# Performance work log

Measured on AMD Instinct MI355X. Metric: run time of the kernel, lower is better.

The kernel has to match this reference:

```python
import jax, jax.numpy as jnp
import numpy as np

N_NODES = 50000
N_EDGES = 1600000
N_GRAPHS = 2048
DIM = 133
EPS = 1e-5


def gcn_conv(x, W, b, row, col, n_nodes):
    # PyG GCNConv: h = x @ W; add self-loops; sym-normalized scatter-add; + b
    h = x @ W  # [N, D]
    loops = jnp.arange(n_nodes, dtype=row.dtype)
    r = jnp.concatenate([row, loops])
    c = jnp.concatenate([col, loops])
    deg = jax.ops.segment_sum(jnp.ones_like(c, dtype=h.dtype), c, num_segments=n_nodes)
    dinv = jnp.where(deg > 0, jax.lax.rsqrt(deg), 0.0)
    norm = dinv[r] * dinv[c]  # [E+N]
    msg = h[r] * norm[:, None]  # gather + scale
    out = jax.ops.segment_sum(msg, c, num_segments=n_nodes)
    return out + b


def batchnorm_eval(x, gamma, beta, rm, rv):
    return (x - rm) * jax.lax.rsqrt(rv + EPS) * gamma + beta


def setup_inputs() -> dict:
    key = jax.random.key(0)
    ks = jax.random.split(key, 8)
    x = jax.random.normal(ks[0], (N_NODES, DIM), dtype=jnp.float32)
    edge_index = jax.random.randint(ks[1], (2, N_EDGES), 0, N_NODES, dtype=jnp.int64)
    batch = jnp.sort(jax.random.randint(ks[2], (N_NODES,), 0, N_GRAPHS, dtype=jnp.int64))
    s = 1.0 / np.sqrt(DIM)
    W1 = jax.random.uniform(ks[3], (DIM, DIM), jnp.float32, -s, s)
    W2 = jax.random.uniform(ks[4], (DIM, DIM), jnp.float32, -s, s)
    b1 = jnp.zeros((DIM,), jnp.float32)
    b2 = jnp.zeros((DIM,), jnp.float32)
    g1 = jnp.ones((DIM,), jnp.float32); beta1 = jnp.zeros((DIM,), jnp.float32)
    rm1 = jax.random.normal(ks[5], (DIM,), jnp.float32) * 0.1
    rv1 = jnp.ones((DIM,), jnp.float32)
    g2 = jnp.ones((DIM,), jnp.float32); beta2 = jnp.zeros((DIM,), jnp.float32)
    rm2 = jax.random.normal(ks[6], (DIM,), jnp.float32) * 0.1
    rv2 = jnp.ones((DIM,), jnp.float32)
    return {"x": x, "edge_index": edge_index, "batch": batch,
            "W1": W1, "b1": b1, "W2": W2, "b2": b2,
            "g1": g1, "beta1": beta1, "rm1": rm1, "rv1": rv1,
            "g2": g2, "beta2": beta2, "rm2": rm2, "rv2": rv2}


def reference(x, edge_index, batch, W1, b1, W2, b2,
              g1, beta1, rm1, rv1, g2, beta2, rm2, rv2):
    row, col = edge_index[0], edge_index[1]
    h = gcn_conv(x, W1, b1, row, col, N_NODES)
    h = jax.nn.relu(h)
    h = batchnorm_eval(h, g1, beta1, rm1, rv1)  # eval-mode BN; dropout is identity in eval
    h = gcn_conv(h, W2, b2, row, col, N_NODES)
    h = jax.nn.relu(h)
    h = batchnorm_eval(h, g2, beta2, rm2, rv2)
    # global mean pool per graph
    sums = jax.ops.segment_sum(h, batch, num_segments=N_GRAPHS)
    cnts = jax.ops.segment_sum(jnp.ones((N_NODES,), h.dtype), batch, num_segments=N_GRAPHS)
    return sums / jnp.maximum(cnts, 1.0)[:, None]
```

## Files before the change

kernel.cpp:

```cpp
#include <hip/hip_runtime.h>

#define N_NODES  50000
#define N_ROWS   50048
#define N_EDGES  1600000
#define N_GRAPHS 2048
#define DIM      133
#define HMSTR    128
#define HTSTR    8
#define YSTR     160
#define EPSV     1e-5f
#define NRANGE   16
#define RSPAN    3125
#define NSLICE   64
#define BUCKCAP  110000
#define EPB      1563
#define NPN      4

typedef __attribute__((ext_vector_type(8))) short bf16x8;
typedef __attribute__((ext_vector_type(4))) float f32x4;

__device__ __forceinline__ float blo(unsigned u) { return __uint_as_float(u << 16); }
__device__ __forceinline__ float bhi(unsigned u) { return __uint_as_float(u & 0xFFFF0000u); }
__device__ __forceinline__ unsigned short f2bf(float x) {
    unsigned v = __float_as_uint(x);
    return (unsigned short)((v + 0x7FFFu + ((v >> 16) & 1u)) >> 16);
}
__device__ __forceinline__ unsigned packbf(float a, float b) {
    return (unsigned)f2bf(a) | ((unsigned)f2bf(b) << 16);
}


__global__ __launch_bounds__(256) void k_part(const int* __restrict__ row,
                                              const int* __restrict__ col,
                                              int* __restrict__ bcnt,
                                              unsigned* __restrict__ buckets)
{
    __shared__ int cnt[NRANGE];
    __shared__ int cur[NRANGE];
    int e0 = blockIdx.x * EPB;
    if (threadIdx.x < NRANGE) cnt[threadIdx.x] = 0;
    __syncthreads();
    int e1 = min(e0 + EPB, N_EDGES);
    for (int e = e0 + threadIdx.x; e < e1; e += 256)
        atomicAdd(&cnt[col[e] / RSPAN], 1);
    __syncthreads();
    if (threadIdx.x < NRANGE)
        cur[threadIdx.x] = atomicAdd(&bcnt[threadIdx.x], cnt[threadIdx.x]);
    __syncthreads();
    for (int e = e0 + threadIdx.x; e < e1; e += 256) {
        int c = col[e];
        int r = c / RSPAN;
        int p = atomicAdd(&cur[r], 1);
        buckets[(size_t)r * BUCKCAP + p] =
            ((unsigned)row[e] << 12) | (unsigned)(c - r * RSPAN);
    }
}

__global__ __launch_bounds__(256) void k_count2(const unsigned* __restrict__ buckets,
                                                const int* __restrict__ bcnt,
                                                int* __restrict__ deg2)
{
    __shared__ int hist[RSPAN];
    int r = blockIdx.x & (NRANGE - 1);
    int s = blockIdx.x >> 4;
    int lo = r * RSPAN;
    for (int i = threadIdx.x; i < RSPAN; i += 256) hist[i] = 0;
    __syncthreads();
    int n = bcnt[r];
    int chunk = (n + NSLICE - 1) / NSLICE;
    int e0 = s * chunk, e1 = min(e0 + chunk, n);
    const unsigned* b = buckets + (size_t)r * BUCKCAP;
    for (int e = e0 + threadIdx.x; e < e1; e += 256)
        atomicAdd(&hist[b[e] & 0xFFFu], 1);
    __syncthreads();
    for (int i = threadIdx.x; i < RSPAN; i += 256)
        deg2[(size_t)s * N_NODES + lo + i] = hist[i];
}

__device__ __forceinline__ void w2bf_one(const float* __restrict__ W,
                                         unsigned short* __restrict__ Wbf, int idx)
{
    int j    = idx & 7;
    int lane = (idx >> 3) & 63;
    int kc   = (idx >> 9) % 5;
    int t    = idx / (8 * 64 * 5);
    int k = kc * 32 + (lane >> 4) * 8 + j;
    int n = t * 16 + (lane & 15);
    float v = (k < DIM && n < DIM) ? W[k * DIM + n] : 0.f;
    Wbf[idx] = f2bf(v);
}

#define X2BF_BLOCKS 15625

__global__ __launch_bounds__(256) void k_prep(const float* __restrict__ x,
                                              unsigned* __restrict__ Abf,
                                              const float* __restrict__ W1,
                                              const float* __restrict__ W2,
                                              unsigned short* __restrict__ Wbf1,
                                              unsigned short* __restrict__ Wbf2,
                                              const int* __restrict__ batch,
                                              float* __restrict__ inv_cnt)
{
    if (blockIdx.x < X2BF_BLOCKS) {
        int idx = blockIdx.x * 256 + threadIdx.x;
        if (idx >= N_NODES * 80) return;
        int r  = idx / 80;
        int c2 = (idx - r * 80) * 2;
        float a = (c2     < DIM) ? x[(size_t)r * DIM + c2]     : 0.f;
        float b = (c2 + 1 < DIM) ? x[(size_t)r * DIM + c2 + 1] : 0.f;
        Abf[idx] = packbf(a, b);
        return;
    }
    int tid = (blockIdx.x - X2BF_BLOCKS) * 256 + threadIdx.x;
    if (tid < 23040) {
        w2bf_one(W1, Wbf1, tid);
    } else if (tid < 46080) {
        w2bf_one(W2, Wbf2, tid - 23040);
    } else if (tid < 46080 + N_GRAPHS) {
        int g = tid - 46080;
        int a0 = 0, b0 = N_NODES;
        while (a0 < b0) { int m = (a0 + b0) >> 1; if (batch[m] < g) a0 = m + 1; else b0 = m; }
        int a1 = a0, b1 = N_NODES;
        while (a1 < b1) { int m = (a1 + b1) >> 1; if (batch[m] < g + 1) a1 = m + 1; else b1 = m; }
        inv_cnt[g] = 1.0f / (float)max(a1 - a0, 1);
    }
}

__global__ __launch_bounds__(256) void k_scan1(const int* __restrict__ deg2,
                                               float* __restrict__ dinv,
                                               int* __restrict__ offs,
                                               int* __restrict__ bsum)
{
    __shared__ int sd[256];
    int t = threadIdx.x;
    int idx = blockIdx.x * 256 + t;
    int v = 0;
    if (idx < N_NODES) {
        for (int s = 0; s < NSLICE; s++) v += deg2[(size_t)s * N_NODES + idx];
        dinv[idx] = rsqrtf((float)v + 1.0f);
    }
    sd[t] = v; __syncthreads();
    for (int o = 1; o < 256; o <<= 1) {
        int add = (t >= o) ? sd[t - o] : 0;
        __syncthreads();
        sd[t] += add;
        __syncthreads();
    }
    if (idx < N_NODES) offs[idx] = sd[t] - v;
    if (t == 255) bsum[blockIdx.x] = sd[255];
}

__global__ __launch_bounds__(256) void k_scan2(const int* __restrict__ bsum,
                                               int* __restrict__ boff, int nb)
{
    __shared__ int sd[256];
    int t = threadIdx.x;
    int v = (t < nb) ? bsum[t] : 0;
    sd[t] = v; __syncthreads();
    for (int o = 1; o < 256; o <<= 1) {
        int add = (t >= o) ? sd[t - o] : 0;
        __syncthreads();
        sd[t] += add;
        __syncthreads();
    }
    boff[t] = sd[t] - v;
}

__global__ __launch_bounds__(256) void k_scan3C(int* __restrict__ offs,
                                                const int* __restrict__ boff,
                                                int* __restrict__ deg2)
{
    int idx = blockIdx.x * 256 + threadIdx.x;
    if (idx < N_NODES) {
        int off = offs[idx] + boff[blockIdx.x];
        offs[idx] = off;
        int run = off;
        for (int s = 0; s < NSLICE; s++) {
            int d = deg2[(size_t)s * N_NODES + idx];
            deg2[(size_t)s * N_NODES + idx] = run;
            run += d;
        }
    } else if (idx == N_NODES) {
        offs[N_NODES] = N_EDGES;
    }
}

__global__ __launch_bounds__(256) void k_fill2(const unsigned* __restrict__ buckets,
                                               const int* __restrict__ bcnt,
                                               const int* __restrict__ offs2,
                                               const float* __restrict__ dinv,
                                               unsigned* __restrict__ csr)
{
    __shared__ int cur[RSPAN];
    int r = blockIdx.x & (NRANGE - 1);
    int s = blockIdx.x >> 4;
    int lo = r * RSPAN;
    for (int i = threadIdx.x; i < RSPAN; i += 256)
        cur[i] = offs2[(size_t)s * N_NODES + lo + i];
    __syncthreads();
    int n = bcnt[r];
    int chunk = (n + NSLICE - 1) / NSLICE;
    int e0 = s * chunk, e1 = min(e0 + chunk, n);
    const unsigned* b = buckets + (size_t)r * BUCKCAP;
    for (int e = e0 + threadIdx.x; e < e1; e += 256) {
        unsigned v = b[e];
        int src = (int)(v >> 12);
        int p = atomicAdd(&cur[v & 0xFFFu], 1);
        csr[p] = ((unsigned)src << 16) | (unsigned)f2bf(dinv[src]);
    }
}

__global__ __launch_bounds__(256) void k_gemm_mfma(const unsigned short* __restrict__ A,
                                                   const unsigned short* __restrict__ Wbf,
                                                   unsigned short* __restrict__ Hmain,
                                                   unsigned short* __restrict__ Htail, int M)
{
    int wave = threadIdx.x >> 6, lane = threadIdx.x & 63;
    int quad = lane >> 4, l16 = lane & 15;
    int m = blockIdx.x * 64 + wave * 16 + l16;

    const bf16x8* Arow = (const bf16x8*)(A + (size_t)m * YSTR);
    const bf16x8* Bq   = (const bf16x8*)Wbf;

    f32x4 acc[9] = {};
#pragma unroll
    for (int kc = 0; kc < 5; kc++) {
        bf16x8 af = Arow[kc * 4 + quad];
#pragma unroll
        for (int t = 0; t < 9; t++) {
            bf16x8 bfr = Bq[(t * 5 + kc) * 64 + lane];
            acc[t] = __builtin_amdgcn_mfma_f32_16x16x32_bf16(af, bfr, acc[t], 0, 0, 0);
        }
    }

    int gr0 = blockIdx.x * 64 + wave * 16 + quad * 4;
#pragma unroll
    for (int t = 0; t < 9; t++) {
        int c = t * 16 + l16;
#pragma unroll
        for (int reg = 0; reg < 4; reg++) {
            int gr = gr0 + reg;
            if (gr < M) {
                if (c < HMSTR) {
                    Hmain[(size_t)gr * HMSTR + c] = f2bf(acc[t][reg]);
                } else if (c < HMSTR + HTSTR) {
                    float v = (c < DIM) ? acc[t][reg] : 0.f;
                    Htail[(size_t)gr * HTSTR + (c - HMSTR)] = f2bf(v);
                }
            }
        }
    }
}


__device__ __forceinline__ void agg_row(const unsigned short* __restrict__ hmain,
                                        const unsigned short* __restrict__ htail,
                                        const int* __restrict__ offs,
                                        const unsigned* __restrict__ csr,
                                        const float* __restrict__ dinv,
                                        const float* __restrict__ bias,
                                        const float* __restrict__ gam,
                                        const float* __restrict__ bet,
                                        const float* __restrict__ rmean,
                                        const float* __restrict__ rvar,
                                        int node, int lane, int l2,
                                        float& va, float& vb, float& ta, float& tb)
{
    const unsigned* hm = (const unsigned*)hmain;
    const unsigned* ht = (const unsigned*)htail;

    float di = dinv[node];
    unsigned pw0 = hm[((size_t)node << 6) + lane];
    unsigned pw1 = ht[((unsigned)node << 2) + l2];
    float2 a0; a0.x = di * blo(pw0); a0.y = di * bhi(pw0);
    float2 a1; a1.x = di * blo(pw1); a1.y = di * bhi(pw1);

    int s0 = offs[node], s1 = offs[node + 1];
    int e = s0;
    for (; e + 8 <= s1; e += 8) {
        unsigned rec[8];
#pragma unroll
        for (int u = 0; u < 8; u++)
            rec[u] = __builtin_amdgcn_readfirstlane(csr[e + u]);
        unsigned q0[8], q1[8];
#pragma unroll
        for (int u = 0; u < 8; u++) {
            const unsigned* hr = hm + ((size_t)(rec[u] >> 16) << 6);
            const unsigned* tr = ht + ((rec[u] >> 16) << 2);
            q0[u] = hr[lane];
            q1[u] = tr[l2];
        }
#pragma unroll
        for (int u = 0; u < 8; u++) {
            float w = __uint_as_float(rec[u] << 16);
            a0.x += w * blo(q0[u]); a0.y += w * bhi(q0[u]);
            a1.x += w * blo(q1[u]); a1.y += w * bhi(q1[u]);
        }
    }
    for (; e < s1; e++) {
        unsigned rec = __builtin_amdgcn_readfirstlane(csr[e]);
        const unsigned* hr = hm + ((size_t)(rec >> 16) << 6);
        const unsigned* tr = ht + ((rec >> 16) << 2);
        float w = __uint_as_float(rec << 16);
        unsigned q0 = hr[lane];
        unsigned q1 = tr[l2];
        a0.x += w * blo(q0); a0.y += w * bhi(q0);
        a1.x += w * blo(q1); a1.y += w * bhi(q1);
    }

    {
        int c = 2 * lane;
        float v = di * a0.x + bias[c];
        v = fmaxf(v, 0.f);
        va = (v - rmean[c]) * (gam[c] * rsqrtf(rvar[c] + EPSV)) + bet[c];
        int c1 = c + 1;
        v = di * a0.y + bias[c1];
        v = fmaxf(v, 0.f);
        vb = (v - rmean[c1]) * (gam[c1] * rsqrtf(rvar[c1] + EPSV)) + bet[c1];
    }
    ta = 0.f; tb = 0.f;
    if (lane < 4) {
        int c = 128 + 2 * l2;
        if (c < DIM) {
            float v = di * a1.x + bias[c];
            v = fmaxf(v, 0.f);
            ta = (v - rmean[c]) * (gam[c] * rsqrtf(rvar[c] + EPSV)) + bet[c];
        }
        int c1 = c + 1;
        if (c1 < DIM) {
            float v = di * a1.y + bias[c1];
            v = fmaxf(v, 0.f);
            tb = (v - rmean[c1]) * (gam[c1] * rsqrtf(rvar[c1] + EPSV)) + bet[c1];
        }
    }
}

template <bool FINAL>
__global__ __launch_bounds__(256) void k_agg(const unsigned short* __restrict__ hmain,
                                             const unsigned short* __restrict__ htail,
                                             const int* __restrict__ offs,
                                             const unsigned* __restrict__ csr,
                                             const float* __restrict__ dinv,
                                             const float* __restrict__ bias,
                                             const float* __restrict__ gam,
                                             const float* __restrict__ bet,
                                             const float* __restrict__ rmean,
                                             const float* __restrict__ rvar,
                                             unsigned short* __restrict__ y,
                                             const int* __restrict__ batch,
                                             const float* __restrict__ inv_cnt,
                                             float* __restrict__ outp)
{
    int lane = threadIdx.x & 63;
    int l2 = lane & 3;

    if (!FINAL) {
        int node = __builtin_amdgcn_readfirstlane(blockIdx.x * 4 + (threadIdx.x >> 6));
        if (node >= N_NODES) return;
        float va, vb, ta, tb;
        agg_row(hmain, htail, offs, csr, dinv, bias, gam, bet, rmean, rvar,
                node, lane, l2, va, vb, ta, tb);
        ((unsigned*)(y + (size_t)node * YSTR))[lane] = packbf(va, vb);
        if (lane < 16)
            ((unsigned*)(y + (size_t)node * YSTR))[64 + lane] =
                (lane < 4) ? packbf(ta, tb) : 0u;
        return;
    }

    int node0 = __builtin_amdgcn_readfirstlane((blockIdx.x * 4 + (threadIdx.x >> 6)) * NPN);
    if (node0 >= N_NODES) return;
    int nend = min(node0 + NPN, N_NODES);

    float p0x = 0.f, p0y = 0.f, p1x = 0.f, p1y = 0.f;
    int curg = batch[node0];

    for (int node = node0; node < nend; node++) {
        int bg = batch[node];
        if (bg != curg) {
            float ic = inv_cnt[curg];
            int c = 2 * lane;
            atomicAdd(&outp[(size_t)curg * DIM + c],     p0x * ic);
            atomicAdd(&outp[(size_t)curg * DIM + c + 1], p0y * ic);
            if (lane < 4) {
                int ct = 128 + 2 * l2;
                if (ct     < DIM) atomicAdd(&outp[(size_t)curg * DIM + ct],     p1x * ic);
                if (ct + 1 < DIM) atomicAdd(&outp[(size_t)curg * DIM + ct + 1], p1y * ic);
            }
            p0x = p0y = p1x = p1y = 0.f;
            curg = bg;
        }
        float va, vb, ta, tb;
        agg_row(hmain, htail, offs, csr, dinv, bias, gam, bet, rmean, rvar,
                node, lane, l2, va, vb, ta, tb);
        p0x += va; p0y += vb; p1x += ta; p1y += tb;
    }
    {
        float ic = inv_cnt[curg];
        int c = 2 * lane;
        atomicAdd(&outp[(size_t)curg * DIM + c],     p0x * ic);
        atomicAdd(&outp[(size_t)curg * DIM + c + 1], p0y * ic);
        if (lane < 4) {
            int ct = 128 + 2 * l2;
            if (ct     < DIM) atomicAdd(&outp[(size_t)curg * DIM + ct],     p1x * ic);
            if (ct + 1 < DIM) atomicAdd(&outp[(size_t)curg * DIM + ct + 1], p1y * ic);
        }
    }
}


extern "C" void kernel_launch(void* const* d_in, const int* in_sizes, int n_in,
                              void* d_out, int out_size, void* d_ws, size_t ws_size,
                              hipStream_t stream)
{
    const float* x   = (const float*)d_in[0];
    const int*   ei  = (const int*)d_in[1];
    const int*   bat = (const int*)d_in[2];
    const float* W1  = (const float*)d_in[3];
    const float* b1  = (const float*)d_in[4];
    const float* W2  = (const float*)d_in[5];
    const float* b2  = (const float*)d_in[6];
    const float* g1  = (const float*)d_in[7];
    const float* be1 = (const float*)d_in[8];
    const float* rm1 = (const float*)d_in[9];
    const float* rv1 = (const float*)d_in[10];
    const float* g2  = (const float*)d_in[11];
    const float* be2 = (const float*)d_in[12];
    const float* rm2 = (const float*)d_in[13];
    const float* rv2 = (const float*)d_in[14];
    float* outp = (float*)d_out;
    char* ws = (char*)d_ws;

    int*   bcnt    = (int*)  (ws + 0);
    int*   offs    = (int*)  (ws + 200000);
    float* dinv    = (float*)(ws + 400016);
    float* inv_cnt = (float*)(ws + 600016);
    int*   bsum    = (int*)  (ws + 608208);
    int*   boff    = (int*)  (ws + 609232);
    unsigned* csr  = (unsigned*)(ws + 610256);
    unsigned short* Wbf1 = (unsigned short*)(ws + 7010256);
    unsigned short* Wbf2 = (unsigned short*)(ws + 7056336);
    unsigned short* Abf  = (unsigned short*)(ws + 7102416);
    unsigned short* Y1   = Abf;
    unsigned short* Hm   = (unsigned short*)(ws + 23118080);
    unsigned short* Ht   = (unsigned short*)(ws + 35930368);
    unsigned* buckets = (unsigned*)(ws + 23118080);
    int*      deg2    = (int*)    (ws + 30158080);

    hipMemsetAsync(bcnt, 0, 64, stream);
    hipMemsetAsync(d_out, 0, (size_t)out_size * 4, stream);

    const int* row = ei;
    const int* col = ei + N_EDGES;

    int nbl = (N_NODES + 255) / 256;

    k_part  <<<dim3(1024), dim3(256), 0, stream>>>(row, col, bcnt, buckets);
    k_prep  <<<dim3(X2BF_BLOCKS + 189), dim3(256), 0, stream>>>(x, (unsigned*)Abf,
                                                                W1, W2, Wbf1, Wbf2,
                                                                bat, inv_cnt);
    k_count2<<<dim3(NSLICE * NRANGE), dim3(256), 0, stream>>>(buckets, bcnt, deg2);
    k_scan1 <<<dim3(nbl), dim3(256), 0, stream>>>(deg2, dinv, offs, bsum);
    k_scan2 <<<dim3(1),   dim3(256), 0, stream>>>(bsum, boff, nbl);
    k_scan3C<<<dim3(nbl), dim3(256), 0, stream>>>(offs, boff, deg2);
    k_fill2 <<<dim3(NSLICE * NRANGE), dim3(256), 0, stream>>>(buckets, bcnt, deg2, dinv, csr);

    int gbl = N_ROWS / 64;
    k_gemm_mfma<<<dim3(gbl), dim3(256), 0, stream>>>(Abf, Wbf1, Hm, Ht, N_NODES);
    k_agg<false><<<dim3(N_NODES / 4), dim3(256), 0, stream>>>(Hm, Ht, offs, csr, dinv,
                                                              b1, g1, be1, rm1, rv1,
                                                              Y1, nullptr, nullptr, nullptr);
    k_gemm_mfma<<<dim3(gbl), dim3(256), 0, stream>>>(Y1, Wbf2, Hm, Ht, N_NODES);
    int fbl = (N_NODES + 4 * NPN - 1) / (4 * NPN);
    k_agg<true><<<dim3(fbl), dim3(256), 0, stream>>>(Hm, Ht, offs, csr, dinv,
                                                     b2, g2, be2, rm2, rv2,
                                                     nullptr, bat, inv_cnt, outp);
}
```

Before: 322.6 us.

## Replace bucketed two-pass CSR build with direct global-atomic degree count and fill

```diff
diff --git a/kernel.cpp b/kernel.cpp
--- a/kernel.cpp
+++ b/kernel.cpp
@@ -9,12 +9,8 @@
 #define HTSTR    8
 #define YSTR     160
 #define EPSV     1e-5f
-#define NRANGE   16
-#define RSPAN    3125
-#define NSLICE   64
-#define BUCKCAP  110000
-#define EPB      1563
 #define NPN      4
+#define EPB2     782
 
 typedef __attribute__((ext_vector_type(8))) short bf16x8;
 typedef __attribute__((ext_vector_type(4))) float f32x4;
@@ -29,53 +25,6 @@
     return (unsigned)f2bf(a) | ((unsigned)f2bf(b) << 16);
 }
 
-
-__global__ __launch_bounds__(256) void k_part(const int* __restrict__ row,
-                                              const int* __restrict__ col,
-                                              int* __restrict__ bcnt,
-                                              unsigned* __restrict__ buckets)
-{
-    __shared__ int cnt[NRANGE];
-    __shared__ int cur[NRANGE];
-    int e0 = blockIdx.x * EPB;
-    if (threadIdx.x < NRANGE) cnt[threadIdx.x] = 0;
-    __syncthreads();
-    int e1 = min(e0 + EPB, N_EDGES);
-    for (int e = e0 + threadIdx.x; e < e1; e += 256)
-        atomicAdd(&cnt[col[e] / RSPAN], 1);
-    __syncthreads();
-    if (threadIdx.x < NRANGE)
-        cur[threadIdx.x] = atomicAdd(&bcnt[threadIdx.x], cnt[threadIdx.x]);
-    __syncthreads();
-    for (int e = e0 + threadIdx.x; e < e1; e += 256) {
-        int c = col[e];
-        int r = c / RSPAN;
-        int p = atomicAdd(&cur[r], 1);
-        buckets[(size_t)r * BUCKCAP + p] =
-            ((unsigned)row[e] << 12) | (unsigned)(c - r * RSPAN);
-    }
-}
-
-__global__ __launch_bounds__(256) void k_count2(const unsigned* __restrict__ buckets,
-                                                const int* __restrict__ bcnt,
-                                                int* __restrict__ deg2)
-{
-    __shared__ int hist[RSPAN];
-    int r = blockIdx.x & (NRANGE - 1);
-    int s = blockIdx.x >> 4;
-    int lo = r * RSPAN;
-    for (int i = threadIdx.x; i < RSPAN; i += 256) hist[i] = 0;
-    __syncthreads();
-    int n = bcnt[r];
-    int chunk = (n + NSLICE - 1) / NSLICE;
-    int e0 = s * chunk, e1 = min(e0 + chunk, n);
-    const unsigned* b = buckets + (size_t)r * BUCKCAP;
-    for (int e = e0 + threadIdx.x; e < e1; e += 256)
-        atomicAdd(&hist[b[e] & 0xFFFu], 1);
-    __syncthreads();
-    for (int i = threadIdx.x; i < RSPAN; i += 256)
-        deg2[(size_t)s * N_NODES + lo + i] = hist[i];
-}
 
 __device__ __forceinline__ void w2bf_one(const float* __restrict__ W,
                                          unsigned short* __restrict__ Wbf, int idx)
@@ -90,7 +39,10 @@
     Wbf[idx] = f2bf(v);
 }
 
-#define X2BF_BLOCKS 15625
+#define PRB_X 15625
+#define PRB_W 189
+#define PRB_Z 1064
+#define PRB_H 2048
 
 __global__ __launch_bounds__(256) void k_prep(const float* __restrict__ x,
                                               unsigned* __restrict__ Abf,
@@ -99,34 +51,50 @@
                                               unsigned short* __restrict__ Wbf1,
                                               unsigned short* __restrict__ Wbf2,
                                               const int* __restrict__ batch,
-                                              float* __restrict__ inv_cnt)
-{
-    if (blockIdx.x < X2BF_BLOCKS) {
-        int idx = blockIdx.x * 256 + threadIdx.x;
+                                              float* __restrict__ inv_cnt,
+                                              const int* __restrict__ col,
+                                              int* __restrict__ deg,
+                                              float* __restrict__ outp)
+{
+    int b = blockIdx.x;
+    if (b < PRB_X) {
+        int idx = b * 256 + threadIdx.x;
         if (idx >= N_NODES * 80) return;
         int r  = idx / 80;
         int c2 = (idx - r * 80) * 2;
         float a = (c2     < DIM) ? x[(size_t)r * DIM + c2]     : 0.f;
-        float b = (c2 + 1 < DIM) ? x[(size_t)r * DIM + c2 + 1] : 0.f;
-        Abf[idx] = packbf(a, b);
+        float bb = (c2 + 1 < DIM) ? x[(size_t)r * DIM + c2 + 1] : 0.f;
+        Abf[idx] = packbf(a, bb);
         return;
     }
-    int tid = (blockIdx.x - X2BF_BLOCKS) * 256 + threadIdx.x;
-    if (tid < 23040) {
-        w2bf_one(W1, Wbf1, tid);
-    } else if (tid < 46080) {
-        w2bf_one(W2, Wbf2, tid - 23040);
-    } else if (tid < 46080 + N_GRAPHS) {
-        int g = tid - 46080;
-        int a0 = 0, b0 = N_NODES;
-        while (a0 < b0) { int m = (a0 + b0) >> 1; if (batch[m] < g) a0 = m + 1; else b0 = m; }
-        int a1 = a0, b1 = N_NODES;
-        while (a1 < b1) { int m = (a1 + b1) >> 1; if (batch[m] < g + 1) a1 = m + 1; else b1 = m; }
-        inv_cnt[g] = 1.0f / (float)max(a1 - a0, 1);
-    }
-}
-
-__global__ __launch_bounds__(256) void k_scan1(const int* __restrict__ deg2,
+    if (b < PRB_X + PRB_W) {
+        int tid = (b - PRB_X) * 256 + threadIdx.x;
+        if (tid < 23040) {
+            w2bf_one(W1, Wbf1, tid);
+        } else if (tid < 46080) {
+            w2bf_one(W2, Wbf2, tid - 23040);
+        } else if (tid < 46080 + N_GRAPHS) {
+            int g = tid - 46080;
+            int a0 = 0, b0 = N_NODES;
+            while (a0 < b0) { int m = (a0 + b0) >> 1; if (batch[m] < g) a0 = m + 1; else b0 = m; }
+            int a1 = a0, b1 = N_NODES;
+            while (a1 < b1) { int m = (a1 + b1) >> 1; if (batch[m] < g + 1) a1 = m + 1; else b1 = m; }
+            inv_cnt[g] = 1.0f / (float)max(a1 - a0, 1);
+        }
+        return;
+    }
+    if (b < PRB_X + PRB_W + PRB_Z) {
+        int i = (b - PRB_X - PRB_W) * 256 + threadIdx.x;
+        outp[i] = 0.f;
+        return;
+    }
+    int e0 = (b - PRB_X - PRB_W - PRB_Z) * EPB2;
+    int e1 = min(e0 + EPB2, N_EDGES);
+    for (int e = e0 + threadIdx.x; e < e1; e += 256)
+        atomicAdd(&deg[col[e]], 1);
+}
+
+__global__ __launch_bounds__(256) void k_scan1(const int* __restrict__ deg,
                                                float* __restrict__ dinv,
                                                int* __restrict__ offs,
                                                int* __restrict__ bsum)
@@ -136,7 +104,7 @@
     int idx = blockIdx.x * 256 + t;
     int v = 0;
     if (idx < N_NODES) {
-        for (int s = 0; s < NSLICE; s++) v += deg2[(size_t)s * N_NODES + idx];
+        v = deg[idx];
         dinv[idx] = rsqrtf((float)v + 1.0f);
     }
     sd[t] = v; __syncthreads();
@@ -150,8 +118,9 @@
     if (t == 255) bsum[blockIdx.x] = sd[255];
 }
 
-__global__ __launch_bounds__(256) void k_scan2(const int* __restrict__ bsum,
-                                               int* __restrict__ boff, int nb)
+__global__ __launch_bounds__(256) void k_scan23(int* __restrict__ offs,
+                                                const int* __restrict__ bsum,
+                                                int* __restrict__ cur, int nb)
 {
     __shared__ int sd[256];
     int t = threadIdx.x;
@@ -163,50 +132,30 @@
         sd[t] += add;
         __syncthreads();
     }
-    boff[t] = sd[t] - v;
-}
-
-__global__ __launch_bounds__(256) void k_scan3C(int* __restrict__ offs,
-                                                const int* __restrict__ boff,
-                                                int* __restrict__ deg2)
-{
-    int idx = blockIdx.x * 256 + threadIdx.x;
+    int boff = sd[blockIdx.x] - ((blockIdx.x < nb) ? bsum[blockIdx.x] : 0);
+    int idx = blockIdx.x * 256 + t;
     if (idx < N_NODES) {
-        int off = offs[idx] + boff[blockIdx.x];
+        int off = offs[idx] + boff;
         offs[idx] = off;
-        int run = off;
-        for (int s = 0; s < NSLICE; s++) {
-            int d = deg2[(size_t)s * N_NODES + idx];
-            deg2[(size_t)s * N_NODES + idx] = run;
-            run += d;
-        }
+        cur[idx] = off;
     } else if (idx == N_NODES) {
         offs[N_NODES] = N_EDGES;
     }
 }
 
-__global__ __launch_bounds__(256) void k_fill2(const unsigned* __restrict__ buckets,
-                                               const int* __restrict__ bcnt,
-                                               const int* __restrict__ offs2,
-                                               const float* __restrict__ dinv,
-                                               unsigned* __restrict__ csr)
-{
-    __shared__ int cur[RSPAN];
-    int r = blockIdx.x & (NRANGE - 1);
-    int s = blockIdx.x >> 4;
-    int lo = r * RSPAN;
-    for (int i = threadIdx.x; i < RSPAN; i += 256)
-        cur[i] = offs2[(size_t)s * N_NODES + lo + i];
-    __syncthreads();
-    int n = bcnt[r];
-    int chunk = (n + NSLICE - 1) / NSLICE;
-    int e0 = s * chunk, e1 = min(e0 + chunk, n);
-    const unsigned* b = buckets + (size_t)r * BUCKCAP;
+__global__ __launch_bounds__(256) void k_fill(const int* __restrict__ row,
+                                              const int* __restrict__ col,
+                                              const float* __restrict__ dinv,
+                                              int* __restrict__ cur,
+                                              unsigned* __restrict__ csr)
+{
+    int e0 = blockIdx.x * EPB2;
+    int e1 = min(e0 + EPB2, N_EDGES);
     for (int e = e0 + threadIdx.x; e < e1; e += 256) {
-        unsigned v = b[e];
-        int src = (int)(v >> 12);
-        int p = atomicAdd(&cur[v & 0xFFFu], 1);
-        csr[p] = ((unsigned)src << 16) | (unsigned)f2bf(dinv[src]);
+        int c = col[e];
+        int r = row[e];
+        int p = atomicAdd(&cur[c], 1);
+        csr[p] = ((unsigned)r << 16) | (unsigned)f2bf(dinv[r]);
     }
 }
 
@@ -430,39 +379,32 @@
     float* outp = (float*)d_out;
     char* ws = (char*)d_ws;
 
-    int*   bcnt    = (int*)  (ws + 0);
+    int*   deg     = (int*)  (ws + 0);
     int*   offs    = (int*)  (ws + 200000);
-    float* dinv    = (float*)(ws + 400016);
-    float* inv_cnt = (float*)(ws + 600016);
-    int*   bsum    = (int*)  (ws + 608208);
-    int*   boff    = (int*)  (ws + 609232);
-    unsigned* csr  = (unsigned*)(ws + 610256);
-    unsigned short* Wbf1 = (unsigned short*)(ws + 7010256);
-    unsigned short* Wbf2 = (unsigned short*)(ws + 7056336);
-    unsigned short* Abf  = (unsigned short*)(ws + 7102416);
+    float* dinv    = (float*)(ws + 400064);
+    int*   cur     = (int*)  (ws + 600064);
+    float* inv_cnt = (float*)(ws + 800064);
+    int*   bsum    = (int*)  (ws + 808256);
+    unsigned* csr  = (unsigned*)(ws + 809280);
+    unsigned short* Wbf1 = (unsigned short*)(ws + 7209280);
+    unsigned short* Wbf2 = (unsigned short*)(ws + 7255360);
+    unsigned short* Abf  = (unsigned short*)(ws + 7301440);
     unsigned short* Y1   = Abf;
-    unsigned short* Hm   = (unsigned short*)(ws + 23118080);
-    unsigned short* Ht   = (unsigned short*)(ws + 35930368);
-    unsigned* buckets = (unsigned*)(ws + 23118080);
-    int*      deg2    = (int*)    (ws + 30158080);
-
-    hipMemsetAsync(bcnt, 0, 64, stream);
-    hipMemsetAsync(d_out, 0, (size_t)out_size * 4, stream);
+    unsigned short* Hm   = (unsigned short*)(ws + 23316992);
+    unsigned short* Ht   = (unsigned short*)(ws + 36129280);
+
+    hipMemsetAsync(deg, 0, 200000, stream);
 
     const int* row = ei;
     const int* col = ei + N_EDGES;
 
     int nbl = (N_NODES + 255) / 256;
 
-    k_part  <<<dim3(1024), dim3(256), 0, stream>>>(row, col, bcnt, buckets);
-    k_prep  <<<dim3(X2BF_BLOCKS + 189), dim3(256), 0, stream>>>(x, (unsigned*)Abf,
-                                                                W1, W2, Wbf1, Wbf2,
-                                                                bat, inv_cnt);
-    k_count2<<<dim3(NSLICE * NRANGE), dim3(256), 0, stream>>>(buckets, bcnt, deg2);
-    k_scan1 <<<dim3(nbl), dim3(256), 0, stream>>>(deg2, dinv, offs, bsum);
-    k_scan2 <<<dim3(1),   dim3(256), 0, stream>>>(bsum, boff, nbl);
-    k_scan3C<<<dim3(nbl), dim3(256), 0, stream>>>(offs, boff, deg2);
-    k_fill2 <<<dim3(NSLICE * NRANGE), dim3(256), 0, stream>>>(buckets, bcnt, deg2, dinv, csr);
+    k_prep  <<<dim3(PRB_X + PRB_W + PRB_Z + PRB_H), dim3(256), 0, stream>>>(
+                x, (unsigned*)Abf, W1, W2, Wbf1, Wbf2, bat, inv_cnt, col, deg, outp);
+    k_scan1 <<<dim3(nbl), dim3(256), 0, stream>>>(deg, dinv, offs, bsum);
+    k_scan23<<<dim3(nbl), dim3(256), 0, stream>>>(offs, bsum, cur, nbl);
+    k_fill  <<<dim3(2048), dim3(256), 0, stream>>>(row, col, dinv, cur, csr);
 
     int gbl = N_ROWS / 64;
     k_gemm_mfma<<<dim3(gbl), dim3(256), 0, stream>>>(Abf, Wbf1, Hm, Ht, N_NODES);
```

Measured after the change: 443.0 us. 37.3% more time.
